# Kernel tuning notes

Hardware: AMD Instinct MI355X
Metric: run time of the kernel (lower is better)

The kernel has to match this reference:

```python
import jax, jax.numpy as jnp
import numpy as np

D = 512
A = 256
MAX_DEPTH = 50.0
ANGLE_RANGE = 60.0
SIGMA = 0.5

ANGLES = jnp.linspace(-ANGLE_RANGE / 2, ANGLE_RANGE / 2, A)  # [A]
DEPTHS = jnp.linspace(0.0, MAX_DEPTH, D)                     # [D]
DEG2RAD = np.float32(np.pi / 180.0)


def _generate_prior(p):
    # p: [B, 3] = [theta_a, d, theta_p]
    d = p[:, 1]        # [B]
    theta_p = p[:, 2]  # [B]
    angle_rad = (theta_p[:, None] + ANGLES[None, :]) * DEG2RAD   # [B, A]
    d_theory = d[:, None] / jnp.cos(angle_rad)                   # [B, A]
    valid = (d_theory > 0.0) & (d_theory < MAX_DEPTH)            # [B, A]
    # Gaussian soft-binning over depth: [B, D, A]
    diff = DEPTHS[None, :, None] - d_theory[:, None, :]
    P = jnp.exp(-(diff * diff) / (2.0 * SIGMA * SIGMA))
    P = jnp.where(valid[:, None, :], P, 0.0)
    # per-column (over depth) normalization, skipping empty columns
    col_sum = P.sum(axis=1, keepdims=True)                       # [B, 1, A]
    denom = jnp.where(col_sum > 0.0, col_sum, 1.0)
    return P / denom


def setup_inputs() -> dict:
    key = jax.random.key(0)
    k1, k2, k3, k4, k5, k6 = jax.random.split(key, 6)
    B = 256

    def make_p(ka, kd, kp):
        theta_a = jax.random.uniform(ka, (B,), minval=-30.0, maxval=30.0)
        d = jax.random.uniform(kd, (B,), minval=1.0, maxval=40.0)
        theta_p = jax.random.uniform(kp, (B,), minval=-10.0, maxval=10.0)
        return jnp.stack([theta_a, d, theta_p], axis=1).astype(jnp.float32)

    return {"p": make_p(k1, k2, k3), "p_calib": make_p(k4, k5, k6)}


def reference(p, p_calib):
    P_d = _generate_prior(p)
    P_c = _generate_prior(p_calib)
    return (P_d, P_c)
```

## Files before the change

### kernel.cpp

```cpp
#include <hip/hip_runtime.h>


#define DD 512
#define AA 256

__global__ __launch_bounds__(256) void prior_kernel(const float* __restrict__ p0,
                                                    const float* __restrict__ p1,
                                                    float* __restrict__ out) {
    const int blk = blockIdx.x;
    const int b   = blk & 255;
    const float* __restrict__ pp = (blk < 256) ? p0 : p1;

    __shared__ __align__(16) float dt_s[AA];
    __shared__ __align__(16) float inv_s[AA];

    const float d  = pp[b * 3 + 1];
    const float th = pp[b * 3 + 2];

    const int t = threadIdx.x;

    {
        const int a = t;
        const float ang = -30.0f + (float)a * (60.0f / 255.0f);
        const float rad = (th + ang) * 0.017453292519943295f;
        float dt = d / cosf(rad);
        const bool valid = (dt > 0.0f) && (dt < 50.0f);
        float sum = 0.0f;
        #pragma unroll 8
        for (int j = 0; j < DD; ++j) {
            const float dep  = (float)j * (50.0f / 511.0f);
            const float diff = dep - dt;
            sum += __expf(-2.0f * diff * diff);
        }
        const float den = (sum > 0.0f) ? sum : 1.0f;
        inv_s[a] = valid ? (1.0f / den) : 0.0f;
        dt_s[a]  = valid ? dt : 1.0e9f;
    }
    __syncthreads();

    const int a4   = (t & 63) * 4;
    const int jblk = t >> 6;
    const float4 dtv = *(const float4*)&dt_s[a4];
    const float4 inv = *(const float4*)&inv_s[a4];

    float* __restrict__ outp = out + (size_t)blk * (DD * AA) + a4;
    const int j0 = jblk * (DD / 4);
    #pragma unroll 4
    for (int j = j0; j < j0 + DD / 4; ++j) {
        const float dep = (float)j * (50.0f / 511.0f);
        float4 v;
        float dx = dep - dtv.x; v.x = __expf(-2.0f * dx * dx) * inv.x;
        float dy = dep - dtv.y; v.y = __expf(-2.0f * dy * dy) * inv.y;
        float dz = dep - dtv.z; v.z = __expf(-2.0f * dz * dz) * inv.z;
        float dw = dep - dtv.w; v.w = __expf(-2.0f * dw * dw) * inv.w;
        *(float4*)(outp + (size_t)j * AA) = v;
    }
}

extern "C" void kernel_launch(void* const* d_in, const int* in_sizes, int n_in,
                              void* d_out, int out_size, void* d_ws, size_t ws_size,
                              hipStream_t stream) {
    const float* p0 = (const float*)d_in[0];
    const float* p1 = (const float*)d_in[1];
    float* out = (float*)d_out;
    prior_kernel<<<dim3(2 * 256), dim3(256), 0, stream>>>(p0, p1, out);
}
```

Before: 262.1 us.

## Split prior into setup and write kernels with finer-grained write blocks

Moves the per-column normalization sum into a separate setup kernel that writes (d_theory, inverse sum) pairs to workspace. The write kernel then launches eight times as many blocks, each covering a 64-row depth chunk, so the output stores spread across more CUs. The sum loop also uses four independent accumulators, and exp is replaced by a direct exp2 with a folded constant. The cost is a second launch and a workspace round-trip.

```diff
diff --git a/kernel.cpp b/kernel.cpp
--- a/kernel.cpp
+++ b/kernel.cpp
@@ -3,56 +3,68 @@
 
 #define DD 512
 #define AA 256
+#define K2 (-2.8853900817779268f)
+#define DSTEP (50.0f / 511.0f)
+#define ASTEP (60.0f / 255.0f)
 
-__global__ __launch_bounds__(256) void prior_kernel(const float* __restrict__ p0,
-                                                    const float* __restrict__ p1,
-                                                    float* __restrict__ out) {
-    const int blk = blockIdx.x;
-    const int b   = blk & 255;
-    const float* __restrict__ pp = (blk < 256) ? p0 : p1;
+__global__ __launch_bounds__(256) void prior_setup(const float* __restrict__ p0,
+                                                   const float* __restrict__ p1,
+                                                   float2* __restrict__ ws) {
+    const int col = blockIdx.x * 256 + threadIdx.x;
+    const int pb  = col >> 8;
+    const int a   = col & 255;
+    const float* __restrict__ pp = (pb < 256) ? (p0 + 3 * pb) : (p1 + 3 * (pb - 256));
+    const float d  = pp[1];
+    const float th = pp[2];
 
-    __shared__ __align__(16) float dt_s[AA];
-    __shared__ __align__(16) float inv_s[AA];
+    const float ang = -30.0f + (float)a * ASTEP;
+    const float rad = (th + ang) * 0.017453292519943295f;
+    const float dt  = d / cosf(rad);
+    const bool valid = (dt > 0.0f) && (dt < 50.0f);
 
-    const float d  = pp[b * 3 + 1];
-    const float th = pp[b * 3 + 2];
+    float s0 = 0.0f, s1 = 0.0f, s2 = 0.0f, s3 = 0.0f;
+    #pragma unroll 4
+    for (int j = 0; j < DD; j += 4) {
+        float x0 = (float)(j + 0) * DSTEP - dt;
+        float x1 = (float)(j + 1) * DSTEP - dt;
+        float x2 = (float)(j + 2) * DSTEP - dt;
+        float x3 = (float)(j + 3) * DSTEP - dt;
+        s0 += __builtin_amdgcn_exp2f(K2 * x0 * x0);
+        s1 += __builtin_amdgcn_exp2f(K2 * x1 * x1);
+        s2 += __builtin_amdgcn_exp2f(K2 * x2 * x2);
+        s3 += __builtin_amdgcn_exp2f(K2 * x3 * x3);
+    }
+    const float sum = (s0 + s1) + (s2 + s3);
+    const float den = (sum > 0.0f) ? sum : 1.0f;
+    float2 r;
+    r.x = valid ? dt : 1.0e9f;
+    r.y = valid ? (1.0f / den) : 0.0f;
+    ws[col] = r;
+}
 
-    const int t = threadIdx.x;
+__global__ __launch_bounds__(256) void prior_write(const float4* __restrict__ ws,
+                                                   float* __restrict__ out) {
+    const int gid   = blockIdx.x;
+    const int pb    = gid >> 3;
+    const int chunk = gid & 7;
+    const int t     = threadIdx.x;
+    const int a4    = (t & 63) * 4;
+    const int jb    = t >> 6;
 
-    {
-        const int a = t;
-        const float ang = -30.0f + (float)a * (60.0f / 255.0f);
-        const float rad = (th + ang) * 0.017453292519943295f;
-        float dt = d / cosf(rad);
-        const bool valid = (dt > 0.0f) && (dt < 50.0f);
-        float sum = 0.0f;
-        #pragma unroll 8
-        for (int j = 0; j < DD; ++j) {
-            const float dep  = (float)j * (50.0f / 511.0f);
-            const float diff = dep - dt;
-            sum += __expf(-2.0f * diff * diff);
-        }
-        const float den = (sum > 0.0f) ? sum : 1.0f;
-        inv_s[a] = valid ? (1.0f / den) : 0.0f;
-        dt_s[a]  = valid ? dt : 1.0e9f;
-    }
-    __syncthreads();
+    const float4 e0 = ws[pb * 128 + (t & 63) * 2];
+    const float4 e1 = ws[pb * 128 + (t & 63) * 2 + 1];
 
-    const int a4   = (t & 63) * 4;
-    const int jblk = t >> 6;
-    const float4 dtv = *(const float4*)&dt_s[a4];
-    const float4 inv = *(const float4*)&inv_s[a4];
-
-    float* __restrict__ outp = out + (size_t)blk * (DD * AA) + a4;
-    const int j0 = jblk * (DD / 4);
-    #pragma unroll 4
-    for (int j = j0; j < j0 + DD / 4; ++j) {
-        const float dep = (float)j * (50.0f / 511.0f);
+    float* __restrict__ outp = out + (size_t)pb * (DD * AA) + a4;
+    const int j0 = chunk * 64 + jb * 16;
+    #pragma unroll
+    for (int i = 0; i < 16; ++i) {
+        const int j = j0 + i;
+        const float dep = (float)j * DSTEP;
         float4 v;
-        float dx = dep - dtv.x; v.x = __expf(-2.0f * dx * dx) * inv.x;
-        float dy = dep - dtv.y; v.y = __expf(-2.0f * dy * dy) * inv.y;
-        float dz = dep - dtv.z; v.z = __expf(-2.0f * dz * dz) * inv.z;
-        float dw = dep - dtv.w; v.w = __expf(-2.0f * dw * dw) * inv.w;
+        float dx = dep - e0.x; v.x = __builtin_amdgcn_exp2f(K2 * dx * dx) * e0.y;
+        float dy = dep - e0.z; v.y = __builtin_amdgcn_exp2f(K2 * dy * dy) * e0.w;
+        float dz = dep - e1.x; v.z = __builtin_amdgcn_exp2f(K2 * dz * dz) * e1.y;
+        float dw = dep - e1.z; v.w = __builtin_amdgcn_exp2f(K2 * dw * dw) * e1.w;
         *(float4*)(outp + (size_t)j * AA) = v;
     }
 }
@@ -63,5 +75,8 @@
     const float* p0 = (const float*)d_in[0];
     const float* p1 = (const float*)d_in[1];
     float* out = (float*)d_out;
-    prior_kernel<<<dim3(2 * 256), dim3(256), 0, stream>>>(p0, p1, out);
+    float2* ws = (float2*)d_ws;
+
+    prior_setup<<<dim3(512), dim3(256), 0, stream>>>(p0, p1, ws);
+    prior_write<<<dim3(512 * 8), dim3(256), 0, stream>>>((const float4*)ws, out);
 }
```

After: 268.7 us. 2.5% more time.
